# Kernel optimization log

Hardware: AMD Instinct MI355X
Metric: run time of the kernel (lower is better)

Reference implementation:

```python
import jax, jax.numpy as jnp
import numpy as np

LMAX = 4  # number of l blocks (lmax+1 in the original)
# segment ids mapping the L2 = sum(2l+1) = 16 spherical components to their l block
SEG = np.repeat(np.arange(LMAX), 2 * np.arange(LMAX) + 1)  # [16]
SEG_ONEHOT = np.eye(LMAX, dtype=np.float32)[SEG]  # [16, LMAX]


def setup_inputs() -> dict:
    key = jax.random.key(0)
    ks = jax.random.split(key, 10)
    b, m, f, k, L2 = 16, 64, 128, 64, 16
    def rnd(kk, shape, scale):
        return jax.random.normal(kk, shape, dtype=jnp.float32) * scale
    return {
        'x': rnd(ks[0], (b, m, f, L2), 1.0),
        'y': rnd(ks[1], (b, m, f, L2), 1.0),
        'wx0': rnd(ks[2], (k, f, f, LMAX), 1.0 / np.sqrt(f * f * LMAX)),
        'wy0': rnd(ks[3], (k, f, f, LMAX), 1.0 / np.sqrt(f * f * LMAX)),
        'wx_mlp': rnd(ks[4], (2, k, k), 1.0 / np.sqrt(k)),
        'bx_mlp': rnd(ks[5], (2, k, k), 0.02),
        'wy_mlp': rnd(ks[6], (2, k, k), 1.0 / np.sqrt(k)),
        'by_mlp': rnd(ks[7], (2, k, k), 0.02),
        'wxf': rnd(ks[8], (LMAX, f, k), 1.0 / np.sqrt(k)),
        'wyf': rnd(ks[9], (LMAX, f, k), 1.0 / np.sqrt(k)),
    }


def reference(x, y, wx0, wy0, wx_mlp, bx_mlp, wy_mlp, by_mlp, wxf, wyf):
    act = jax.nn.silu
    S = jnp.asarray(SEG_ONEHOT)  # [L2, lmax]
    # outer product of y and x features, segment-summed over each l block:
    # mix[b,m,fy,fx,l] = sum_c y[b,m,fy,c] * x[b,m,fx,c] * S[c,l]
    mix = jnp.einsum('bmfc,bmgc,cl->bmfgl', y, x, S)  # [b,m,f,f,lmax]
    mx = jnp.einsum('bmfgl,kfgl->bmk', mix, wx0)
    my = jnp.einsum('bmfgl,kfgl->bmk', mix, wy0)
    for i in range(wx_mlp.shape[0]):  # the n_mlp-1 used MLP stages
        mx = act(jnp.einsum('bmk,kl->bml', mx, wx_mlp[i]) + bx_mlp[i])
        my = act(jnp.einsum('bmk,kl->bml', my, wy_mlp[i]) + by_mlp[i])
    mx = act(jnp.einsum('bmk,lfk->bmfl', mx, wxf))  # [b,m,f,lmax]
    my = act(jnp.einsum('bmk,lfk->bmfl', my, wyf))
    # broadcast each l gate over its 2l+1 components (repeat == gather by SEG)
    seg = jnp.asarray(SEG)
    res = mx[..., seg] * x + my[..., seg] * y  # [b,m,f,L2]
    return res
```

## Files before the change

kernel.cpp:

```cpp
#include <hip/hip_runtime.h>
#include <stdint.h>


#define AS1 __attribute__((address_space(1)))
#define AS3 __attribute__((address_space(3)))

typedef __bf16 bf16x8 __attribute__((ext_vector_type(8)));
typedef float f32x4 __attribute__((ext_vector_type(4)));

__device__ __forceinline__ uint16_t f2b(float f) {
  uint32_t u = __float_as_uint(f);
  u += 0x7fffu + ((u >> 16) & 1u);
  return (uint16_t)(u >> 16);
}

#if __has_builtin(__builtin_amdgcn_fdot2_f32_bf16)
typedef __bf16 bf16x2 __attribute__((ext_vector_type(2)));
__device__ __forceinline__ float dot2b(uint32_t a, uint32_t b, float c) {
  union { uint32_t u; bf16x2 v; } ua, ub;
  ua.u = a; ub.u = b;
  return __builtin_amdgcn_fdot2_f32_bf16(ua.v, ub.v, c, false);
}
#else
__device__ __forceinline__ float dot2b(uint32_t a, uint32_t b, float c) {
  float a0 = __uint_as_float(a << 16), a1 = __uint_as_float(a & 0xffff0000u);
  float b0 = __uint_as_float(b << 16), b1 = __uint_as_float(b & 0xffff0000u);
  return c + a0 * b0 + a1 * b1;
}
#endif

__global__ __launch_bounds__(256) void convert_all(
    const float* __restrict__ wx0, const float* __restrict__ wy0,
    const float* __restrict__ x, const float* __restrict__ y,
    const float* __restrict__ wxf, const float* __restrict__ wyf,
    uint16_t* __restrict__ Wb2, uint16_t* __restrict__ xb,
    uint16_t* __restrict__ ybT, float* __restrict__ wfT) {
  int bid = blockIdx.x, tid = threadIdx.x;
  if (bid < 4096) {
    int c = bid * 256 + tid;
    int fb = c >> 16;
    int rem = c & 65535;
    int fy = rem >> 9;
    int rem2 = rem & 511;
    int n = rem2 >> 2, pos = rem2 & 3;
    int slot = pos ^ ((n >> 1) & 3);
    int k = n & 63;
    const float* src = (n < 64 ? wx0 : wy0) +
        ((size_t)(k * 128 + fy) * 512 + fb * 32 + slot * 8);
    float4 v0 = *(const float4*)src;
    float4 v1 = *(const float4*)(src + 4);
    uint32_t o0 = (uint32_t)f2b(v0.x) | ((uint32_t)f2b(v0.y) << 16);
    uint32_t o1 = (uint32_t)f2b(v0.z) | ((uint32_t)f2b(v0.w) << 16);
    uint32_t o2 = (uint32_t)f2b(v1.x) | ((uint32_t)f2b(v1.y) << 16);
    uint32_t o3 = (uint32_t)f2b(v1.z) | ((uint32_t)f2b(v1.w) << 16);
    *(uint4*)(Wb2 + (size_t)c * 8) = make_uint4(o0, o1, o2, o3);
    return;
  }
  if (bid >= 6144) {
    int base = (bid - 6144) * 2048 + tid * 8;
#pragma unroll
    for (int ii = 0; ii < 8; ++ii) {
      int idx = base + ii;
      int side = idx >> 15, rem = idx & 32767;
      int k = rem >> 9, l = (rem >> 7) & 3, f = rem & 127;
      const float* src = side ? wyf : wxf;
      wfT[idx] = src[((size_t)l * 128 + f) * 64 + k];
    }
    return;
  }
  if (bid < 5120) {
    size_t i = ((size_t)(bid - 4096) * 256 + tid) * 8;
    const float* s = x + i;
    float4 v0 = *(const float4*)s;
    float4 v1 = *(const float4*)(s + 4);
    uint32_t o0 = (uint32_t)f2b(v0.x) | ((uint32_t)f2b(v0.y) << 16);
    uint32_t o1 = (uint32_t)f2b(v0.z) | ((uint32_t)f2b(v0.w) << 16);
    uint32_t o2 = (uint32_t)f2b(v1.x) | ((uint32_t)f2b(v1.y) << 16);
    uint32_t o3 = (uint32_t)f2b(v1.z) | ((uint32_t)f2b(v1.w) << 16);
    *(uint4*)(xb + i) = make_uint4(o0, o1, o2, o3);
    return;
  }
  {
    int c = (bid - 5120) * 256 + tid;
    int half = c & 1, fy = (c >> 1) & 127, m = c >> 8;
    const float* s = y + (size_t)c * 8;
    float4 v0 = *(const float4*)s;
    float4 v1 = *(const float4*)(s + 4);
    uint32_t o0 = (uint32_t)f2b(v0.x) | ((uint32_t)f2b(v0.y) << 16);
    uint32_t o1 = (uint32_t)f2b(v0.z) | ((uint32_t)f2b(v0.w) << 16);
    uint32_t o2 = (uint32_t)f2b(v1.x) | ((uint32_t)f2b(v1.y) << 16);
    uint32_t o3 = (uint32_t)f2b(v1.z) | ((uint32_t)f2b(v1.w) << 16);
    *(uint4*)(ybT + ((size_t)fy * 1024 + m) * 16 + half * 8) =
        make_uint4(o0, o1, o2, o3);
  }
}

__device__ __forceinline__ void gload_lds16(const void* g, void* l) {
  __builtin_amdgcn_global_load_lds((const AS1 uint32_t*)g, (AS3 uint32_t*)l, 16, 0, 0);
}

#define SB0 __builtin_amdgcn_sched_barrier(0)
#define PIPE_BAR(N) \
  asm volatile("s_waitcnt vmcnt(" #N ") lgkmcnt(0)\n\ts_barrier" ::: "memory")

__global__ __launch_bounds__(256, 4) void fused_gemm(
    const uint16_t* __restrict__ xb, const uint16_t* __restrict__ ybT,
    const uint16_t* __restrict__ Wb2, float* __restrict__ Cpart) {
  __shared__ __align__(16) uint16_t sA[2][64 * 32];
  __shared__ __align__(16) uint16_t sB[3][128 * 32];

  int tid = threadIdx.x;
  int w = tid >> 6, lane = tid & 63;
  int g_id = blockIdx.x;
  int fb = g_id >> 2, fyg = g_id & 3;
  int FB = fb * 8;
  int fy0 = fyg * 32;
  int m0 = blockIdx.y * 64;
  int r = lane & 15, q = lane >> 4;
  int wm = w >> 1, wn = w & 1;
  int m_loc = tid & 63, quarter = tid >> 6;

  uint32_t xr[16];
  {
    const uint16_t* xp0 = xb + (size_t)(m0 + m_loc) * 2048 + (FB + quarter * 2) * 16;
#pragma unroll
    for (int j = 0; j < 4; ++j) {
      uint4 v = *(const uint4*)(xp0 + j * 8);
      xr[j * 4 + 0] = v.x; xr[j * 4 + 1] = v.y;
      xr[j * 4 + 2] = v.z; xr[j * 4 + 3] = v.w;
    }
  }

  f32x4 zero = {0.f, 0.f, 0.f, 0.f};
  f32x4 acc[2][4];
#pragma unroll
  for (int i = 0; i < 2; ++i)
#pragma unroll
    for (int j = 0; j < 4; ++j) acc[i][j] = zero;

  auto issueB = [&](uint16_t* dstB, int t) {
    size_t base = (size_t)(fb * 128 + fy0 + t) * 4096;
#pragma unroll
    for (int jj = 0; jj < 2; ++jj) {
      int blk = w * 2 + jj;
      gload_lds16(Wb2 + base + blk * 512 + lane * 8, dstB + blk * 512);
    }
  };

  const uint16_t* ybase = ybT + (size_t)(m0 + m_loc) * 16;

  auto computeG = [&](uint4 ya, uint4 yc, float* gg) {
    uint32_t yp[8] = {ya.x, ya.y, ya.z, ya.w, yc.x, yc.y, yc.z, yc.w};
    uint32_t yl0 = yp[0] & 0xffffu, yh0 = yp[0] & 0xffff0000u;
    uint32_t yl4 = yp[4] & 0xffffu, yh4 = yp[4] & 0xffff0000u;
#pragma unroll
    for (int fxp = 0; fxp < 2; ++fxp) {
      const uint32_t* xp = xr + fxp * 8;
      gg[fxp * 4 + 0] = dot2b(xp[0], yl0, 0.f);
      gg[fxp * 4 + 1] = dot2b(xp[1], yp[1], dot2b(xp[0], yh0, 0.f));
      gg[fxp * 4 + 2] = dot2b(xp[4], yl4,
                         dot2b(xp[3], yp[3], dot2b(xp[2], yp[2], 0.f)));
      gg[fxp * 4 + 3] = dot2b(xp[7], yp[7], dot2b(xp[6], yp[6],
                         dot2b(xp[5], yp[5], dot2b(xp[4], yh4, 0.f))));
    }
  };
  auto writeA = [&](uint16_t* dstA, const float* gg) {
    uint32_t o[4];
#pragma unroll
    for (int p = 0; p < 4; ++p)
      o[p] = (__float_as_uint(gg[2 * p]) >> 16) |
             (__float_as_uint(gg[2 * p + 1]) & 0xffff0000u);
    int pos = quarter ^ ((m_loc >> 1) & 3);
    *(uint4*)(dstA + m_loc * 32 + pos * 8) = make_uint4(o[0], o[1], o[2], o[3]);
  };

  uint16_t *pAc = sA[0], *pAn = sA[1];
  uint16_t *pBread = sB[0], *pBmid = sB[1], *pBissue = sB[2];

  float gg[8];
  issueB(pBread, 0);
  issueB(pBmid, 1);
  SB0;
  uint4 yev0, yev1, yod0, yod1;
  {
    const uint16_t* yp0 = ybase + (size_t)fy0 * 16384;
    uint4 t0a = *(const uint4*)yp0;
    uint4 t0b = *(const uint4*)(yp0 + 8);
    computeG(t0a, t0b, gg);
    writeA(pAc, gg);
    yev0 = *(const uint4*)(ybase + (size_t)(fy0 + 1) * 16384);
    yev1 = *(const uint4*)(ybase + (size_t)(fy0 + 1) * 16384 + 8);
    yod0 = *(const uint4*)(ybase + (size_t)(fy0 + 2) * 16384);
    yod1 = *(const uint4*)(ybase + (size_t)(fy0 + 2) * 16384 + 8);
  }
  SB0;
  PIPE_BAR(4);

  auto body = [&](int t, uint4& y0_, uint4& y1_) {
    if (t <= 29) issueB(pBissue, t + 2);
    SB0;
    bf16x8 a[2], b[4];
#pragma unroll
    for (int i = 0; i < 2; ++i) {
      int row = wm * 32 + i * 16 + r;
      int pos = q ^ ((row >> 1) & 3);
      a[i] = *(const bf16x8*)&pAc[row * 32 + pos * 8];
    }
#pragma unroll
    for (int j = 0; j < 4; ++j) {
      int row = wn * 64 + j * 16 + r;
      int pos = q ^ ((row >> 1) & 3);
      b[j] = *(const bf16x8*)&pBread[row * 32 + pos * 8];
    }
    if (t < 31) {
      computeG(y0_, y1_, gg);
      writeA(pAn, gg);
    }
    if (t <= 28) {
      y0_ = *(const uint4*)(ybase + (size_t)(fy0 + t + 3) * 16384);
      y1_ = *(const uint4*)(ybase + (size_t)(fy0 + t + 3) * 16384 + 8);
    }
    SB0;
    __builtin_amdgcn_s_setprio(1);
#pragma unroll
    for (int i = 0; i < 2; ++i)
#pragma unroll
      for (int j = 0; j < 4; ++j)
        acc[i][j] = __builtin_amdgcn_mfma_f32_16x16x32_bf16(a[i], b[j], acc[i][j], 0, 0, 0);
    __builtin_amdgcn_s_setprio(0);

    if (t <= 28)      PIPE_BAR(6);
    else if (t == 29) PIPE_BAR(4);
    else if (t == 30) PIPE_BAR(0);

    uint16_t* tp;
    tp = pAc; pAc = pAn; pAn = tp;
    tp = pBread; pBread = pBmid; pBmid = pBissue; pBissue = tp;
  };

  for (int t = 0; t < 32; t += 2) {
    body(t, yev0, yev1);
    body(t + 1, yod0, yod1);
  }

#pragma unroll
  for (int i = 0; i < 2; ++i)
#pragma unroll
    for (int j = 0; j < 4; ++j)
#pragma unroll
      for (int reg = 0; reg < 4; ++reg) {
        int mm = m0 + wm * 32 + i * 16 + q * 4 + reg;
        int nn = wn * 64 + j * 16 + r;
        Cpart[((size_t)mm * 64 + g_id) * 128 + nn] = acc[i][j][reg];
      }
}

__global__ __launch_bounds__(256) void finish_kernel(
    const float* __restrict__ x, const float* __restrict__ y,
    const float* __restrict__ wx_mlp, const float* __restrict__ bx_mlp,
    const float* __restrict__ wy_mlp, const float* __restrict__ by_mlp,
    const float* __restrict__ wfT,
    const float* __restrict__ Cpart, float* __restrict__ out) {
  const int seg[16] = {0,1,1,1,2,2,2,2,2,3,3,3,3,3,3,3};
  __shared__ float sred[256];
  __shared__ float sm[128];
  __shared__ float sg[2][128][4];
  int t = threadIdx.x;
  int bm = blockIdx.x;
  int mi = bm & 63;

  {
    int col = t & 127, hh = t >> 7;
    const float* cp = Cpart + ((size_t)bm * 64 + hh * 32) * 128 + col;
    float s = 0.f;
#pragma unroll 8
    for (int sp = 0; sp < 32; ++sp)
      s += cp[(size_t)sp * 128];
    sred[t] = s;
  }
  __syncthreads();
  if (t < 128) sm[t] = sred[t] + sred[t + 128];
  __syncthreads();

  for (int st = 0; st < 2; ++st) {
    float v = 0.f;
    if (t < 128) {
      int side = t >> 6, j = t & 63;
      const float* wmlp = side ? wy_mlp : wx_mlp;
      const float* bmlp = side ? by_mlp : bx_mlp;
      const float* mv = sm + side * 64;
#pragma unroll 8
      for (int k = 0; k < 64; ++k)
        v += mv[k] * wmlp[(st * 64 + k) * 64 + j];
      v += bmlp[(st * 64 + mi) * 64 + j];
      v = v / (1.f + __expf(-v));
    }
    __syncthreads();
    if (t < 128) sm[t] = v;
    __syncthreads();
  }

  {
    int side = t >> 7, f = t & 127;
    const float* base = wfT + side * 32768;
    const float* mv = sm + side * 64;
    float gg[4] = {0.f, 0.f, 0.f, 0.f};
#pragma unroll 8
    for (int k = 0; k < 64; ++k) {
      float m2 = mv[k];
#pragma unroll
      for (int l = 0; l < 4; ++l)
        gg[l] += m2 * base[(k * 4 + l) * 128 + f];
    }
#pragma unroll
    for (int l = 0; l < 4; ++l)
      sg[side][f][l] = gg[l] / (1.f + __expf(-gg[l]));
  }
  __syncthreads();

  {
    int f = t >> 1, half = t & 1;
    size_t base = ((size_t)bm * 128 + f) * 16 + half * 8;
    float4 xa = *(const float4*)(x + base), xb4 = *(const float4*)(x + base + 4);
    float4 ya = *(const float4*)(y + base), yb4 = *(const float4*)(y + base + 4);
    float xv[8] = {xa.x, xa.y, xa.z, xa.w, xb4.x, xb4.y, xb4.z, xb4.w};
    float yv[8] = {ya.x, ya.y, ya.z, ya.w, yb4.x, yb4.y, yb4.z, yb4.w};
    float o[8];
#pragma unroll
    for (int ii = 0; ii < 8; ++ii) {
      int c = half * 8 + ii;
      o[ii] = sg[0][f][seg[c]] * xv[ii] + sg[1][f][seg[c]] * yv[ii];
    }
    *(float4*)(out + base)     = make_float4(o[0], o[1], o[2], o[3]);
    *(float4*)(out + base + 4) = make_float4(o[4], o[5], o[6], o[7]);
  }
}

extern "C" void kernel_launch(void* const* d_in, const int* in_sizes, int n_in,
                              void* d_out, int out_size, void* d_ws, size_t ws_size,
                              hipStream_t stream) {
  const float* x      = (const float*)d_in[0];
  const float* y      = (const float*)d_in[1];
  const float* wx0    = (const float*)d_in[2];
  const float* wy0    = (const float*)d_in[3];
  const float* wx_mlp = (const float*)d_in[4];
  const float* bx_mlp = (const float*)d_in[5];
  const float* wy_mlp = (const float*)d_in[6];
  const float* by_mlp = (const float*)d_in[7];
  const float* wxf    = (const float*)d_in[8];
  const float* wyf    = (const float*)d_in[9];
  float* out = (float*)d_out;

  uint16_t* Wb2   = (uint16_t*)d_ws;
  uint16_t* xb    = (uint16_t*)((char*)d_ws + (size_t)16777216);
  uint16_t* ybT   = (uint16_t*)((char*)d_ws + (size_t)20971520);
  float*    Cpart = (float*)((char*)d_ws + (size_t)25165824);
  float*    wfT   = (float*)((char*)d_ws + (size_t)58720256);

  convert_all<<<6176, 256, 0, stream>>>(wx0, wy0, x, y, wxf, wyf, Wb2, xb, ybT, wfT);
  fused_gemm<<<dim3(64, 16), 256, 0, stream>>>(xb, ybT, Wb2, Cpart);
  finish_kernel<<<1024, 256, 0, stream>>>(x, y, wx_mlp, bx_mlp, wy_mlp, by_mlp,
                                          wfT, Cpart, out);
}
```

Baseline: 165.8 us.

## Reduce split-K partials via atomics and coalesce weight reads in conversion

The GEMM no longer writes 64 per-block partial sums to a large scratch buffer for the finish kernel to reduce. It atomically adds its results into a small zeroed buffer, which the convert kernel now clears. The weight-conversion kernel is also reindexed so it reads the fp32 weights sequentially and scatters the bf16 chunks into the swizzled layout, rather than gathering them. This trades the partial-buffer write and read traffic for float atomic contention and a nondeterministic summation order.

```diff
diff --git a/kernel.cpp b/kernel.cpp
--- a/kernel.cpp
+++ b/kernel.cpp
@@ -34,26 +34,35 @@
     const float* __restrict__ x, const float* __restrict__ y,
     const float* __restrict__ wxf, const float* __restrict__ wyf,
     uint16_t* __restrict__ Wb2, uint16_t* __restrict__ xb,
-    uint16_t* __restrict__ ybT, float* __restrict__ wfT) {
+    uint16_t* __restrict__ ybT, float* __restrict__ wfT,
+    float* __restrict__ Cred) {
   int bid = blockIdx.x, tid = threadIdx.x;
   if (bid < 4096) {
     int c = bid * 256 + tid;
-    int fb = c >> 16;
-    int rem = c & 65535;
-    int fy = rem >> 9;
-    int rem2 = rem & 511;
-    int n = rem2 >> 2, pos = rem2 & 3;
-    int slot = pos ^ ((n >> 1) & 3);
-    int k = n & 63;
-    const float* src = (n < 64 ? wx0 : wy0) +
-        ((size_t)(k * 128 + fy) * 512 + fb * 32 + slot * 8);
+    int side = c >> 19;
+    int us = c & 524287;
+    int fxh = us & 63;
+    int fy = (us >> 6) & 127;
+    int k = us >> 13;
+    int n = side * 64 + k;
+    int fb = fxh >> 2, q = fxh & 3;
+    int pos = q ^ ((n >> 1) & 3);
+    size_t chunk = (((size_t)fb * 128 + fy) * 128 + n) * 4 + pos;
+    const float* src = (side ? wy0 : wx0) + (size_t)us * 8;
     float4 v0 = *(const float4*)src;
     float4 v1 = *(const float4*)(src + 4);
     uint32_t o0 = (uint32_t)f2b(v0.x) | ((uint32_t)f2b(v0.y) << 16);
     uint32_t o1 = (uint32_t)f2b(v0.z) | ((uint32_t)f2b(v0.w) << 16);
     uint32_t o2 = (uint32_t)f2b(v1.x) | ((uint32_t)f2b(v1.y) << 16);
     uint32_t o3 = (uint32_t)f2b(v1.z) | ((uint32_t)f2b(v1.w) << 16);
-    *(uint4*)(Wb2 + (size_t)c * 8) = make_uint4(o0, o1, o2, o3);
+    *(uint4*)(Wb2 + chunk * 8) = make_uint4(o0, o1, o2, o3);
+    return;
+  }
+  if (bid >= 6176) {
+    int idx = (bid - 6176) * 2048 + tid * 8;
+    float4 z = make_float4(0.f, 0.f, 0.f, 0.f);
+    *(float4*)(Cred + idx) = z;
+    *(float4*)(Cred + idx + 4) = z;
     return;
   }
   if (bid >= 6144) {
@@ -105,7 +114,7 @@
 
 __global__ __launch_bounds__(256, 4) void fused_gemm(
     const uint16_t* __restrict__ xb, const uint16_t* __restrict__ ybT,
-    const uint16_t* __restrict__ Wb2, float* __restrict__ Cpart) {
+    const uint16_t* __restrict__ Wb2, float* __restrict__ Cred) {
   __shared__ __align__(16) uint16_t sA[2][64 * 32];
   __shared__ __align__(16) uint16_t sB[3][128 * 32];
 
@@ -251,7 +260,7 @@
       for (int reg = 0; reg < 4; ++reg) {
         int mm = m0 + wm * 32 + i * 16 + q * 4 + reg;
         int nn = wn * 64 + j * 16 + r;
-        Cpart[((size_t)mm * 64 + g_id) * 128 + nn] = acc[i][j][reg];
+        unsafeAtomicAdd(&Cred[(size_t)mm * 128 + nn], acc[i][j][reg]);
       }
 }
 
@@ -260,26 +269,15 @@
     const float* __restrict__ wx_mlp, const float* __restrict__ bx_mlp,
     const float* __restrict__ wy_mlp, const float* __restrict__ by_mlp,
     const float* __restrict__ wfT,
-    const float* __restrict__ Cpart, float* __restrict__ out) {
+    const float* __restrict__ Cred, float* __restrict__ out) {
   const int seg[16] = {0,1,1,1,2,2,2,2,2,3,3,3,3,3,3,3};
-  __shared__ float sred[256];
   __shared__ float sm[128];
   __shared__ float sg[2][128][4];
   int t = threadIdx.x;
   int bm = blockIdx.x;
   int mi = bm & 63;
 
-  {
-    int col = t & 127, hh = t >> 7;
-    const float* cp = Cpart + ((size_t)bm * 64 + hh * 32) * 128 + col;
-    float s = 0.f;
-#pragma unroll 8
-    for (int sp = 0; sp < 32; ++sp)
-      s += cp[(size_t)sp * 128];
-    sred[t] = s;
-  }
-  __syncthreads();
-  if (t < 128) sm[t] = sred[t] + sred[t + 128];
+  if (t < 128) sm[t] = Cred[(size_t)bm * 128 + t];
   __syncthreads();
 
   for (int st = 0; st < 2; ++st) {
@@ -354,11 +352,12 @@
   uint16_t* Wb2   = (uint16_t*)d_ws;
   uint16_t* xb    = (uint16_t*)((char*)d_ws + (size_t)16777216);
   uint16_t* ybT   = (uint16_t*)((char*)d_ws + (size_t)20971520);
-  float*    Cpart = (float*)((char*)d_ws + (size_t)25165824);
-  float*    wfT   = (float*)((char*)d_ws + (size_t)58720256);
-
-  convert_all<<<6176, 256, 0, stream>>>(wx0, wy0, x, y, wxf, wyf, Wb2, xb, ybT, wfT);
-  fused_gemm<<<dim3(64, 16), 256, 0, stream>>>(xb, ybT, Wb2, Cpart);
+  float*    Cred  = (float*)((char*)d_ws + (size_t)25165824);
+  float*    wfT   = (float*)((char*)d_ws + (size_t)25690112);
+
+  convert_all<<<6240, 256, 0, stream>>>(wx0, wy0, x, y, wxf, wyf,
+                                        Wb2, xb, ybT, wfT, Cred);
+  fused_gemm<<<dim3(64, 16), 256, 0, stream>>>(xb, ybT, Wb2, Cred);
   finish_kernel<<<1024, 256, 0, stream>>>(x, y, wx_mlp, bx_mlp, wy_mlp, by_mlp,
-                                          wfT, Cpart, out);
-}
+                                          wfT, Cred, out);
+}
```

Result: slower. 173.2 us (+4.5%).

## Build MFMA A-fragments in registers and coalesce weight conversion reads

Applied to the files above, without the earlier changes.

The fused GEMM now computes the y⊗x segment-sum products directly into the MFMA A-operand registers of each lane instead of writing them to a double-buffered LDS tile and reading them back, removing the sA buffer, its LDS traffic, and one barrier dependency. Each lane now loads x for its own fragment rows and doubles its y loads, so each wave repeats A-side dot products, raising VALU work and register use. The weight conversion kernel now reads the source weights sequentially and scatters to the swizzled layout, making global reads coalesced at the cost of scattered writes. Wait counts in the pipeline barriers are adjusted for the extra y loads in flight.

```diff
diff --git a/kernel.cpp b/kernel.cpp
--- a/kernel.cpp
+++ b/kernel.cpp
@@ -38,22 +38,23 @@
   int bid = blockIdx.x, tid = threadIdx.x;
   if (bid < 4096) {
     int c = bid * 256 + tid;
-    int fb = c >> 16;
-    int rem = c & 65535;
-    int fy = rem >> 9;
-    int rem2 = rem & 511;
-    int n = rem2 >> 2, pos = rem2 & 3;
-    int slot = pos ^ ((n >> 1) & 3);
-    int k = n & 63;
-    const float* src = (n < 64 ? wx0 : wy0) +
-        ((size_t)(k * 128 + fy) * 512 + fb * 32 + slot * 8);
+    int side = c >> 19;
+    int us = c & 524287;
+    int fxh = us & 63;
+    int fy = (us >> 6) & 127;
+    int k = us >> 13;
+    int n = side * 64 + k;
+    int fb = fxh >> 2, q = fxh & 3;
+    int pos = q ^ ((n >> 1) & 3);
+    size_t chunk = (((size_t)fb * 128 + fy) * 128 + n) * 4 + pos;
+    const float* src = (side ? wy0 : wx0) + (size_t)us * 8;
     float4 v0 = *(const float4*)src;
     float4 v1 = *(const float4*)(src + 4);
     uint32_t o0 = (uint32_t)f2b(v0.x) | ((uint32_t)f2b(v0.y) << 16);
     uint32_t o1 = (uint32_t)f2b(v0.z) | ((uint32_t)f2b(v0.w) << 16);
     uint32_t o2 = (uint32_t)f2b(v1.x) | ((uint32_t)f2b(v1.y) << 16);
     uint32_t o3 = (uint32_t)f2b(v1.z) | ((uint32_t)f2b(v1.w) << 16);
-    *(uint4*)(Wb2 + (size_t)c * 8) = make_uint4(o0, o1, o2, o3);
+    *(uint4*)(Wb2 + chunk * 8) = make_uint4(o0, o1, o2, o3);
     return;
   }
   if (bid >= 6144) {
@@ -106,7 +107,6 @@
 __global__ __launch_bounds__(256, 4) void fused_gemm(
     const uint16_t* __restrict__ xb, const uint16_t* __restrict__ ybT,
     const uint16_t* __restrict__ Wb2, float* __restrict__ Cpart) {
-  __shared__ __align__(16) uint16_t sA[2][64 * 32];
   __shared__ __align__(16) uint16_t sB[3][128 * 32];
 
   int tid = threadIdx.x;
@@ -118,16 +118,17 @@
   int m0 = blockIdx.y * 64;
   int r = lane & 15, q = lane >> 4;
   int wm = w >> 1, wn = w & 1;
-  int m_loc = tid & 63, quarter = tid >> 6;
-
-  uint32_t xr[16];
-  {
-    const uint16_t* xp0 = xb + (size_t)(m0 + m_loc) * 2048 + (FB + quarter * 2) * 16;
-#pragma unroll
-    for (int j = 0; j < 4; ++j) {
-      uint4 v = *(const uint4*)(xp0 + j * 8);
-      xr[j * 4 + 0] = v.x; xr[j * 4 + 1] = v.y;
-      xr[j * 4 + 2] = v.z; xr[j * 4 + 3] = v.w;
+
+  uint32_t xreg[2][16];
+#pragma unroll
+  for (int i = 0; i < 2; ++i) {
+    const uint16_t* xp0 =
+        xb + (size_t)(m0 + wm * 32 + i * 16 + r) * 2048 + (FB + 2 * q) * 16;
+#pragma unroll
+    for (int j2 = 0; j2 < 4; ++j2) {
+      uint4 v = *(const uint4*)(xp0 + j2 * 8);
+      xreg[i][j2 * 4 + 0] = v.x; xreg[i][j2 * 4 + 1] = v.y;
+      xreg[i][j2 * 4 + 2] = v.z; xreg[i][j2 * 4 + 3] = v.w;
     }
   }
 
@@ -147,100 +148,85 @@
     }
   };
 
-  const uint16_t* ybase = ybT + (size_t)(m0 + m_loc) * 16;
-
-  auto computeG = [&](uint4 ya, uint4 yc, float* gg) {
-    uint32_t yp[8] = {ya.x, ya.y, ya.z, ya.w, yc.x, yc.y, yc.z, yc.w};
+  const uint16_t* ybase0 = ybT + (size_t)(m0 + wm * 32 + r) * 16;
+  const uint16_t* ybase1 = ybase0 + 256;
+
+  auto packA = [&](const uint32_t* xp16, const uint32_t* yp, uint32_t* afu) {
     uint32_t yl0 = yp[0] & 0xffffu, yh0 = yp[0] & 0xffff0000u;
     uint32_t yl4 = yp[4] & 0xffffu, yh4 = yp[4] & 0xffff0000u;
 #pragma unroll
     for (int fxp = 0; fxp < 2; ++fxp) {
-      const uint32_t* xp = xr + fxp * 8;
-      gg[fxp * 4 + 0] = dot2b(xp[0], yl0, 0.f);
-      gg[fxp * 4 + 1] = dot2b(xp[1], yp[1], dot2b(xp[0], yh0, 0.f));
-      gg[fxp * 4 + 2] = dot2b(xp[4], yl4,
-                         dot2b(xp[3], yp[3], dot2b(xp[2], yp[2], 0.f)));
-      gg[fxp * 4 + 3] = dot2b(xp[7], yp[7], dot2b(xp[6], yp[6],
-                         dot2b(xp[5], yp[5], dot2b(xp[4], yh4, 0.f))));
+      const uint32_t* xp = xp16 + fxp * 8;
+      float g0 = dot2b(xp[0], yl0, 0.f);
+      float g1 = dot2b(xp[1], yp[1], dot2b(xp[0], yh0, 0.f));
+      float g2 = dot2b(xp[4], yl4,
+                  dot2b(xp[3], yp[3], dot2b(xp[2], yp[2], 0.f)));
+      float g3 = dot2b(xp[7], yp[7], dot2b(xp[6], yp[6],
+                  dot2b(xp[5], yp[5], dot2b(xp[4], yh4, 0.f))));
+      afu[fxp * 2 + 0] = (__float_as_uint(g0) >> 16) |
+                         (__float_as_uint(g1) & 0xffff0000u);
+      afu[fxp * 2 + 1] = (__float_as_uint(g2) >> 16) |
+                         (__float_as_uint(g3) & 0xffff0000u);
     }
   };
-  auto writeA = [&](uint16_t* dstA, const float* gg) {
-    uint32_t o[4];
-#pragma unroll
-    for (int p = 0; p < 4; ++p)
-      o[p] = (__float_as_uint(gg[2 * p]) >> 16) |
-             (__float_as_uint(gg[2 * p + 1]) & 0xffff0000u);
-    int pos = quarter ^ ((m_loc >> 1) & 3);
-    *(uint4*)(dstA + m_loc * 32 + pos * 8) = make_uint4(o[0], o[1], o[2], o[3]);
-  };
-
-  uint16_t *pAc = sA[0], *pAn = sA[1];
+
   uint16_t *pBread = sB[0], *pBmid = sB[1], *pBissue = sB[2];
 
-  float gg[8];
   issueB(pBread, 0);
   issueB(pBmid, 1);
   SB0;
-  uint4 yev0, yev1, yod0, yod1;
-  {
-    const uint16_t* yp0 = ybase + (size_t)fy0 * 16384;
-    uint4 t0a = *(const uint4*)yp0;
-    uint4 t0b = *(const uint4*)(yp0 + 8);
-    computeG(t0a, t0b, gg);
-    writeA(pAc, gg);
-    yev0 = *(const uint4*)(ybase + (size_t)(fy0 + 1) * 16384);
-    yev1 = *(const uint4*)(ybase + (size_t)(fy0 + 1) * 16384 + 8);
-    yod0 = *(const uint4*)(ybase + (size_t)(fy0 + 2) * 16384);
-    yod1 = *(const uint4*)(ybase + (size_t)(fy0 + 2) * 16384 + 8);
+  uint4 e00, e01, e10, e11, o00, o01, o10, o11;
+  {
+    const uint16_t* p0 = ybase0 + (size_t)fy0 * 16384;
+    const uint16_t* p1 = ybase1 + (size_t)fy0 * 16384;
+    e00 = *(const uint4*)p0;            e01 = *(const uint4*)(p0 + 8);
+    e10 = *(const uint4*)p1;            e11 = *(const uint4*)(p1 + 8);
+    o00 = *(const uint4*)(p0 + 16384);  o01 = *(const uint4*)(p0 + 16392);
+    o10 = *(const uint4*)(p1 + 16384);  o11 = *(const uint4*)(p1 + 16392);
   }
   SB0;
-  PIPE_BAR(4);
-
-  auto body = [&](int t, uint4& y0_, uint4& y1_) {
+  PIPE_BAR(10);
+
+  auto body = [&](int t, uint4& y00, uint4& y01, uint4& y10, uint4& y11) {
     if (t <= 29) issueB(pBissue, t + 2);
     SB0;
-    bf16x8 a[2], b[4];
-#pragma unroll
-    for (int i = 0; i < 2; ++i) {
-      int row = wm * 32 + i * 16 + r;
-      int pos = q ^ ((row >> 1) & 3);
-      a[i] = *(const bf16x8*)&pAc[row * 32 + pos * 8];
-    }
+    union { uint32_t u[4]; bf16x8 v; } af0, af1;
+    {
+      uint32_t yp[8] = {y00.x, y00.y, y00.z, y00.w, y01.x, y01.y, y01.z, y01.w};
+      packA(xreg[0], yp, af0.u);
+    }
+    {
+      uint32_t yp[8] = {y10.x, y10.y, y10.z, y10.w, y11.x, y11.y, y11.z, y11.w};
+      packA(xreg[1], yp, af1.u);
+    }
+    if (t <= 29) {
+      const uint16_t* p0 = ybase0 + (size_t)(fy0 + t + 2) * 16384;
+      const uint16_t* p1 = ybase1 + (size_t)(fy0 + t + 2) * 16384;
+      y00 = *(const uint4*)p0;  y01 = *(const uint4*)(p0 + 8);
+      y10 = *(const uint4*)p1;  y11 = *(const uint4*)(p1 + 8);
+    }
+    SB0;
+    __builtin_amdgcn_s_setprio(1);
 #pragma unroll
     for (int j = 0; j < 4; ++j) {
       int row = wn * 64 + j * 16 + r;
       int pos = q ^ ((row >> 1) & 3);
-      b[j] = *(const bf16x8*)&pBread[row * 32 + pos * 8];
-    }
-    if (t < 31) {
-      computeG(y0_, y1_, gg);
-      writeA(pAn, gg);
-    }
-    if (t <= 28) {
-      y0_ = *(const uint4*)(ybase + (size_t)(fy0 + t + 3) * 16384);
-      y1_ = *(const uint4*)(ybase + (size_t)(fy0 + t + 3) * 16384 + 8);
-    }
-    SB0;
-    __builtin_amdgcn_s_setprio(1);
-#pragma unroll
-    for (int i = 0; i < 2; ++i)
-#pragma unroll
-      for (int j = 0; j < 4; ++j)
-        acc[i][j] = __builtin_amdgcn_mfma_f32_16x16x32_bf16(a[i], b[j], acc[i][j], 0, 0, 0);
+      bf16x8 bj = *(const bf16x8*)&pBread[row * 32 + pos * 8];
+      acc[0][j] = __builtin_amdgcn_mfma_f32_16x16x32_bf16(af0.v, bj, acc[0][j], 0, 0, 0);
+      acc[1][j] = __builtin_amdgcn_mfma_f32_16x16x32_bf16(af1.v, bj, acc[1][j], 0, 0, 0);
+    }
     __builtin_amdgcn_s_setprio(0);
 
-    if (t <= 28)      PIPE_BAR(6);
-    else if (t == 29) PIPE_BAR(4);
-    else if (t == 30) PIPE_BAR(0);
+    if (t <= 29)      PIPE_BAR(10);
+    else if (t == 30) PIPE_BAR(4);
 
     uint16_t* tp;
-    tp = pAc; pAc = pAn; pAn = tp;
     tp = pBread; pBread = pBmid; pBmid = pBissue; pBissue = tp;
   };
 
   for (int t = 0; t < 32; t += 2) {
-    body(t, yev0, yev1);
-    body(t + 1, yod0, yod1);
+    body(t, e00, e01, e10, e11);
+    body(t + 1, o00, o01, o10, o11);
   }
 
 #pragma unroll
```

New measurement: 281.1 us. 69.5% more time.
